# Kernel tuning notes

Measured on AMD Instinct MI355X. Metric: run time of the kernel, lower is better.

## Reference

```python
import jax, jax.numpy as jnp
import numpy as np

# Longformer-base-4096 dims; attention_window=128 -> one-sided window 64
B, S, D, H, L, F, V, NUM_LABELS = 1, 4096, 768, 12, 12, 3072, 50265, 100
DH = D // H
W = 64            # one-sided sliding window
NC = S // W       # number of query chunks
EPS = 1e-5
SCALE = float(1.0 / np.sqrt(DH))


def layer_norm(x, s, b):
    m = jnp.mean(x, axis=-1, keepdims=True)
    v = jnp.mean(jnp.square(x - m), axis=-1, keepdims=True)
    return (x - m) * jax.lax.rsqrt(v + EPS) * s + b


def heads(x):  # [B,S,D] -> [B,H,S,DH]
    return x.reshape(B, S, H, DH).transpose(0, 2, 1, 3)


def chunk3(t):  # [B,H,S,DH] -> [B,H,NC,3W,DH]: key blocks c-1,c,c+1 per query chunk c
    tp = jnp.pad(t, ((0, 0), (0, 0), (W, W), (0, 0)))
    tb = tp.reshape(B, H, NC + 2, W, DH)
    return jnp.concatenate([tb[:, :, i:i + NC] for i in range(3)], axis=3)


def _forward(input_ids, attention_mask, emb_tok, emb_pos, ln_emb_scale, ln_emb_bias,
             Wq, bq, Wk, bk, Wv, bv, Wqg, bqg, Wkg, bkg, Wvg, bvg, Wo, bo,
             ln1_scale, ln1_bias, Wf1, bf1, Wf2, bf2, ln2_scale, ln2_bias, Wc, bc):
    am = attention_mask > 0                      # [B,S]
    x = layer_norm(emb_tok[input_ids] + emb_pos[None, :, :], ln_emb_scale, ln_emb_bias)

    # static sliding-window masks, shared by all layers
    qi = jnp.arange(W)[:, None]
    kj = jnp.arange(3 * W)[None, :]
    band = (kj >= qi) & (kj <= qi + 2 * W)       # |key - query| <= W within a chunk triple
    kvalid = am & (jnp.arange(S)[None, :] > 0)   # global token (pos 0) excluded from window
    kp = jnp.pad(kvalid, ((0, 0), (W, W))).reshape(B, NC + 2, W)
    kmask = jnp.concatenate([kp[:, i:i + NC] for i in range(3)], axis=2)   # [B,NC,3W]
    win_mask = band[None, None, None] & kmask[:, None, :, None, :]         # [B,1,NC,W,3W]

    def layer(x, p):
        (wq, bq_, wk, bk_, wv, bv_, wqg, bqg_, wkg, bkg_, wvg, bvg_, wo, bo_,
         l1s, l1b, wf1, bf1_, wf2, bf2_, l2s, l2b) = p
        q = heads(x @ wq + bq_) * SCALE
        k = heads(x @ wk + bk_)
        v = heads(x @ wv + bv_)
        qc = q.reshape(B, H, NC, W, DH)
        k3, v3 = chunk3(k), chunk3(v)
        sc = jnp.einsum('bhcqd,bhckd->bhcqk', qc, k3)          # [B,H,NC,W,3W]
        sc = jnp.where(win_mask, sc, -1e9)
        # every token also attends to the global CLS key (standard K/V of pos 0)
        sg = jnp.einsum('bhsd,bhd->bhs', q, k[:, :, 0]).reshape(B, H, NC, W, 1)
        probs = jax.nn.softmax(jnp.concatenate([sg, sc], axis=-1), axis=-1)
        pg, pl = probs[..., 0], probs[..., 1:]
        ctx = jnp.einsum('bhcqk,bhckd->bhcqd', pl, v3).reshape(B, H, S, DH)
        ctx = ctx + pg.reshape(B, H, S, 1) * v[:, :, :1]
        # global token attends to everything with its own (global) projections
        qg = heads(x @ wqg + bqg_)[:, :, 0] * SCALE            # [B,H,DH]
        kg = heads(x @ wkg + bkg_)
        vg = heads(x @ wvg + bvg_)
        sgl = jnp.where(am[:, None, :], jnp.einsum('bhd,bhjd->bhj', qg, kg), -1e9)
        ctx0 = jnp.einsum('bhj,bhjd->bhd', jax.nn.softmax(sgl, axis=-1), vg)
        ctx = ctx.at[:, :, 0].set(ctx0)
        attn = ctx.transpose(0, 2, 1, 3).reshape(B, S, D) @ wo + bo_
        x1 = layer_norm(x + attn, l1s, l1b)
        h = jax.nn.gelu(x1 @ wf1 + bf1_, approximate=False)
        return layer_norm(x1 + h @ wf2 + bf2_, l2s, l2b), None

    params = (Wq, bq, Wk, bk, Wv, bv, Wqg, bqg, Wkg, bkg, Wvg, bvg, Wo, bo,
              ln1_scale, ln1_bias, Wf1, bf1, Wf2, bf2, ln2_scale, ln2_bias)
    x, _ = jax.lax.scan(layer, x, params)
    return x[:, 0] @ Wc + bc                                   # [B, NUM_LABELS]


def setup_inputs():
    key = jax.random.key(0)
    ks = jax.random.split(key, 40)
    it = iter(range(40))
    nrm = lambda shape: jax.random.normal(ks[next(it)], shape, dtype=jnp.float32) * 0.02
    z = lambda shape: jnp.zeros(shape, jnp.float32)
    o = lambda shape: jnp.ones(shape, jnp.float32)
    return {
        'input_ids': jax.random.randint(ks[next(it)], (B, S), 0, V, dtype=jnp.int32),
        'attention_mask': jnp.ones((B, S), dtype=jnp.int32),
        'emb_tok': nrm((V, D)), 'emb_pos': nrm((S, D)),
        'ln_emb_scale': o((D,)), 'ln_emb_bias': z((D,)),
        'Wq': nrm((L, D, D)), 'bq': z((L, D)),
        'Wk': nrm((L, D, D)), 'bk': z((L, D)),
        'Wv': nrm((L, D, D)), 'bv': z((L, D)),
        'Wqg': nrm((L, D, D)), 'bqg': z((L, D)),
        'Wkg': nrm((L, D, D)), 'bkg': z((L, D)),
        'Wvg': nrm((L, D, D)), 'bvg': z((L, D)),
        'Wo': nrm((L, D, D)), 'bo': z((L, D)),
        'ln1_scale': o((L, D)), 'ln1_bias': z((L, D)),
        'Wf1': nrm((L, D, F)), 'bf1': z((L, F)),
        'Wf2': nrm((L, F, D)), 'bf2': z((L, D)),
        'ln2_scale': o((L, D)), 'ln2_bias': z((L, D)),
        'Wc': nrm((D, NUM_LABELS)), 'bc': z((NUM_LABELS,)),
    }


def reference(input_ids, attention_mask, emb_tok, emb_pos, ln_emb_scale, ln_emb_bias,
              Wq, bq, Wk, bk, Wv, bv, Wqg, bqg, Wkg, bkg, Wvg, bvg, Wo, bo,
              ln1_scale, ln1_bias, Wf1, bf1, Wf2, bf2, ln2_scale, ln2_bias, Wc, bc):
    return _forward(input_ids, attention_mask, emb_tok, emb_pos, ln_emb_scale, ln_emb_bias,
                    Wq, bq, Wk, bk, Wv, bv, Wqg, bqg, Wkg, bkg, Wvg, bvg, Wo, bo,
                    ln1_scale, ln1_bias, Wf1, bf1, Wf2, bf2, ln2_scale, ln2_bias, Wc, bc)
```

## Files before the change

kernel.cpp:

```cpp
#include <hip/hip_runtime.h>
#include <hip/hip_bf16.h>

typedef unsigned short u16;
typedef __attribute__((ext_vector_type(8))) short bf16x8;
typedef __attribute__((ext_vector_type(4))) float f32x4;

constexpr int S = 4096, D = 768, H = 12, NL = 12, F = 3072, NLAB = 100, DH = 64;
constexpr int NQKV = 3840;
constexpr float SCALE = 0.125f;
constexpr float EPS = 1e-5f;

__device__ __forceinline__ float bits2f(u16 u) {
  union { unsigned int i; float f; } x; x.i = ((unsigned int)u) << 16; return x.f;
}
__device__ __forceinline__ u16 f2bbits(float f) {
  union { float f; unsigned int i; } x; x.f = f;
  return (u16)((x.i + 0x7FFFu + ((x.i >> 16) & 1u)) >> 16);
}
__device__ __forceinline__ float rdw(const void* p, size_t i, int isf32) {
  return isf32 ? ((const float*)p)[i] : bits2f(((const u16*)p)[i]);
}
__device__ __forceinline__ void gload16(const void* g, void* l) {
  __builtin_amdgcn_global_load_lds(
      (const __attribute__((address_space(1))) void*)g,
      (__attribute__((address_space(3))) void*)l, 16, 0, 0);
}

__global__ void detect_k(const void* lns, int* flag) {
  *flag = (*(const unsigned int*)lns == 0x3F800000u) ? 1 : 0;
}

struct PrepArgs {
  const void *Wq, *Wk, *Wv, *Wkg, *Wvg, *Wo, *Wqg, *Wf1, *Wf2;
  const void *bq, *bk, *bv, *bkg, *bvg, *bo, *bqg, *bf1, *bf2;
  u16 *wt_qkv, *wt_o, *wt_qg, *wt_f1, *wt_f2;
  float* biasb;
  const int* flag;
};

__global__ __launch_bounds__(256) void prep_all(PrepArgs a)
{
  const int l = blockIdx.x / 8676;
  const int b = blockIdx.x % 8676;
  const int t = threadIdx.x;
  const int isf32 = *a.flag;
  const size_t oDD = (size_t)l * D * D, oDF = (size_t)l * D * F;
  const size_t oD = (size_t)l * D, oF = (size_t)l * F;
  u16* wqkv = a.wt_qkv + (size_t)l * NQKV * D;
  u16* wo   = a.wt_o   + (size_t)l * D * D;
  u16* wqg  = a.wt_qg  + (size_t)l * D * D;
  u16* wf1  = a.wt_f1  + (size_t)l * F * D;
  u16* wf2  = a.wt_f2  + (size_t)l * D * F;
  float* bb = a.biasb + (size_t)l * 9216;

  if (b < 8640) {
    __shared__ float tile[32][33];
    const void* src; size_t soff; int N, ld, rowoff, n0, k0;
    u16* dst; float scl = 1.f;
    if (b < 4032) {
      const int m = b / 576, ti = b - m * 576;
      soff = oDD; N = D; ld = D; rowoff = 0;
      switch (m) {
        case 0:  src = a.Wq;  dst = wqkv; scl = SCALE;  break;
        case 1:  src = a.Wk;  dst = wqkv; rowoff = 768; break;
        case 2:  src = a.Wv;  dst = wqkv; rowoff = 1536; break;
        case 3:  src = a.Wkg; dst = wqkv; rowoff = 2304; break;
        case 4:  src = a.Wvg; dst = wqkv; rowoff = 3072; break;
        case 5:  src = a.Wo;  dst = wo;   break;
        default: src = a.Wqg; dst = wqg;  scl = SCALE;  break;
      }
      n0 = (ti % 24) * 32; k0 = (ti / 24) * 32;
    } else if (b < 6336) {
      const int ti = b - 4032;
      src = a.Wf1; soff = oDF; N = F; dst = wf1; rowoff = 0; ld = D;
      n0 = (ti % 96) * 32; k0 = (ti / 96) * 32;
    } else {
      const int ti = b - 6336;
      src = a.Wf2; soff = oDF; N = D; dst = wf2; rowoff = 0; ld = F;
      n0 = (ti % 24) * 32; k0 = (ti / 24) * 32;
    }
    const int r = t >> 3, cc = (t & 7) << 2;
    const size_t si = soff + (size_t)(k0 + r) * N + n0 + cc;
    if (isf32) {
      const float4 v = *reinterpret_cast<const float4*>(&((const float*)src)[si]);
      tile[r][cc] = v.x * scl; tile[r][cc+1] = v.y * scl;
      tile[r][cc+2] = v.z * scl; tile[r][cc+3] = v.w * scl;
    } else {
      const ushort4 v = *reinterpret_cast<const ushort4*>(&((const u16*)src)[si]);
      tile[r][cc] = bits2f(v.x) * scl; tile[r][cc+1] = bits2f(v.y) * scl;
      tile[r][cc+2] = bits2f(v.z) * scl; tile[r][cc+3] = bits2f(v.w) * scl;
    }
    __syncthreads();
    const ushort4 ov = make_ushort4(f2bbits(tile[cc+0][r]), f2bbits(tile[cc+1][r]),
                                    f2bbits(tile[cc+2][r]), f2bbits(tile[cc+3][r]));
    *reinterpret_cast<ushort4*>(&dst[(size_t)(rowoff + n0 + r) * ld + k0 + cc]) = ov;
  } else {
    const int i = (b - 8640) * 256 + t;
    float v;
    if      (i < 768)  v = rdw(a.bq,  oD + i,        isf32) * SCALE;
    else if (i < 1536) v = rdw(a.bk,  oD + i - 768,  isf32);
    else if (i < 2304) v = rdw(a.bv,  oD + i - 1536, isf32);
    else if (i < 3072) v = rdw(a.bkg, oD + i - 2304, isf32);
    else if (i < 3840) v = rdw(a.bvg, oD + i - 3072, isf32);
    else if (i < 4608) v = rdw(a.bo,  oD + i - 3840, isf32);
    else if (i < 7680) v = rdw(a.bf1, oF + i - 4608, isf32);
    else if (i < 8448) v = rdw(a.bf2, oD + i - 7680, isf32);
    else               v = rdw(a.bqg, oD + i - 8448, isf32) * SCALE;
    bb[i] = v;
  }
}

template<int BN, int SPLITK>
__global__ __launch_bounds__(256) void mfma_gemm(
    const u16* __restrict__ A, const u16* __restrict__ BT,
    const float* __restrict__ bias,
    float* __restrict__ Cf, u16* __restrict__ Cb,
    int M, int N, int K, int act)
{
  constexpr int BM = 128, BK = 32;
  constexpr int WN = BN / 2;
  constexpr int NR = WN / 16;
  __shared__ u16 As[BM * BK];
  __shared__ u16 Bs[BN * BK];
  const int t = threadIdx.x;
  const int wid = t >> 6, lane = t & 63;
  const int wr = wid >> 1, wc = wid & 1;
  const int m0 = blockIdx.y * BM, n0 = blockIdx.x * BN;
  const int z = (SPLITK > 1) ? blockIdx.z : 0;
  const int kLen = K / SPLITK;
  const int k0 = z * kLen;
  const int l_row = lane >> 2;
  const int l_kc = (lane & 3) << 3;

  f32x4 acc[4][NR];
#pragma unroll
  for (int m = 0; m < 4; ++m)
#pragma unroll
    for (int n = 0; n < NR; ++n)
      acc[m][n] = (f32x4){0.f, 0.f, 0.f, 0.f};

  const int frow = lane & 15;
  const int fkb = (lane >> 4) << 3;

  for (int kt = k0; kt < k0 + kLen; kt += BK) {
#pragma unroll
    for (int i = 0; i < 2; ++i) {
      const int ch = wid * 2 + i;
      gload16(&A[(size_t)(m0 + ch * 16 + l_row) * K + kt + l_kc], &As[ch * 512]);
    }
#pragma unroll
    for (int i = 0; i < BN / 64; ++i) {
      const int ch = wid * (BN / 64) + i;
      gload16(&BT[(size_t)(n0 + ch * 16 + l_row) * K + kt + l_kc], &Bs[ch * 512]);
    }
    __syncthreads();
    bf16x8 af[4], bfr[NR];
#pragma unroll
    for (int m = 0; m < 4; ++m)
      af[m] = *reinterpret_cast<const bf16x8*>(&As[(wr * 64 + m * 16 + frow) * BK + fkb]);
#pragma unroll
    for (int n = 0; n < NR; ++n)
      bfr[n] = *reinterpret_cast<const bf16x8*>(&Bs[(wc * WN + n * 16 + frow) * BK + fkb]);
#pragma unroll
    for (int m = 0; m < 4; ++m)
#pragma unroll
      for (int n = 0; n < NR; ++n)
        acc[m][n] = __builtin_amdgcn_mfma_f32_16x16x32_bf16(af[m], bfr[n], acc[m][n], 0, 0, 0);
    __syncthreads();
  }

  float* Cp = (SPLITK > 1) ? (Cf + (size_t)z * M * N) : Cf;
  const int crow = (lane >> 4) << 2;
  const int ccol = lane & 15;
#pragma unroll
  for (int m = 0; m < 4; ++m) {
#pragma unroll
    for (int n = 0; n < NR; ++n) {
      const int gc = n0 + wc * WN + n * 16 + ccol;
      const float bv = (z == 0) ? bias[gc] : 0.f;
#pragma unroll
      for (int r = 0; r < 4; ++r) {
        const int gr = m0 + wr * 64 + m * 16 + crow + r;
        float x = acc[m][n][r] + bv;
        if (SPLITK == 1 && act) x = 0.5f * x * (1.0f + erff(x * 0.70710678118654752f));
        if (Cp) Cp[(size_t)gr * N + gc] = x;
        if (SPLITK == 1 && Cb) Cb[(size_t)gr * N + gc] = f2bbits(x);
      }
    }
  }
}

__global__ void embed_k(const int* __restrict__ ids, const void* __restrict__ tok,
                        const void* __restrict__ pos, float* __restrict__ out,
                        const int* __restrict__ flag)
{
  const int isf32 = *flag;
  const int s = blockIdx.x, t = threadIdx.x;
  const int id = ids[s];
  for (int c = t; c < D; c += 256)
    out[(size_t)s * D + c] = rdw(tok, (size_t)id * D + c, isf32) + rdw(pos, (size_t)s * D + c, isf32);
}

__global__ __launch_bounds__(256) void ln_res_k(
    const float* __restrict__ Ain,
    const float* __restrict__ P0, const float* __restrict__ P1,
    const float* __restrict__ P2, const float* __restrict__ P3,
    const void* __restrict__ g, size_t goff, const void* __restrict__ b, size_t boff,
    float* __restrict__ Out, u16* __restrict__ Outb, const int* __restrict__ flag)
{
  const int isf32 = *flag;
  const int w = threadIdx.x >> 6, lane = threadIdx.x & 63;
  const int r = blockIdx.x * 4 + w;
  const size_t rb = (size_t)r * D;
  float v[12];
  float ls = 0.f;
#pragma unroll
  for (int j = 0; j < 3; ++j) {
    const int c = lane * 4 + j * 256;
    float4 x = *reinterpret_cast<const float4*>(&Ain[rb + c]);
    if (P0) { const float4 p = *reinterpret_cast<const float4*>(&P0[rb + c]);
              x.x += p.x; x.y += p.y; x.z += p.z; x.w += p.w; }
    if (P1) { const float4 p = *reinterpret_cast<const float4*>(&P1[rb + c]);
              x.x += p.x; x.y += p.y; x.z += p.z; x.w += p.w; }
    if (P2) { const float4 p = *reinterpret_cast<const float4*>(&P2[rb + c]);
              x.x += p.x; x.y += p.y; x.z += p.z; x.w += p.w; }
    if (P3) { const float4 p = *reinterpret_cast<const float4*>(&P3[rb + c]);
              x.x += p.x; x.y += p.y; x.z += p.z; x.w += p.w; }
    v[j*4+0] = x.x; v[j*4+1] = x.y; v[j*4+2] = x.z; v[j*4+3] = x.w;
    ls += x.x + x.y + x.z + x.w;
  }
#pragma unroll
  for (int off = 32; off; off >>= 1) ls += __shfl_xor(ls, off);
  const float mean = ls * (1.0f / D);
  float lv = 0.f;
#pragma unroll
  for (int e = 0; e < 12; ++e) { const float dd = v[e] - mean; lv += dd * dd; }
#pragma unroll
  for (int off = 32; off; off >>= 1) lv += __shfl_xor(lv, off);
  const float rstd = rsqrtf(lv * (1.0f / D) + EPS);
#pragma unroll
  for (int j = 0; j < 3; ++j) {
    const int c = lane * 4 + j * 256;
    float o[4];
#pragma unroll
    for (int e = 0; e < 4; ++e)
      o[e] = (v[j*4+e] - mean) * rstd * rdw(g, goff + c + e, isf32) + rdw(b, boff + c + e, isf32);
    *reinterpret_cast<float4*>(&Out[rb + c]) = make_float4(o[0], o[1], o[2], o[3]);
    if (Outb)
      *reinterpret_cast<ushort4*>(&Outb[rb + c]) =
          make_ushort4(f2bbits(o[0]), f2bbits(o[1]), f2bbits(o[2]), f2bbits(o[3]));
  }
}

__global__ __launch_bounds__(256) void qg_gemv(
    const u16* __restrict__ Xb, const u16* __restrict__ WgT,
    const float* __restrict__ biasb, float* __restrict__ QG)
{
  const int wid = threadIdx.x >> 6, lane = threadIdx.x & 63;
  const int o = blockIdx.x * 4 + wid;
  float a = 0.f;
#pragma unroll
  for (int j = 0; j < 12; ++j) {
    const int k = j * 64 + lane;
    a += bits2f(Xb[k]) * bits2f(WgT[(size_t)o * 768 + k]);
  }
#pragma unroll
  for (int off = 32; off; off >>= 1) a += __shfl_xor(a, off);
  if (lane == 0) QG[o] = a + biasb[8448 + o];
}

__global__ __launch_bounds__(256) void win_attn3(
    const u16* __restrict__ QKV, const int* __restrict__ am, u16* __restrict__ CTXb)
{
  __shared__ u16 Ql[64 * 64];
  __shared__ u16 Kl[224 * 64];
  __shared__ u16 Vt[64 * 232];
  __shared__ int kwin[224];
  const int c = blockIdx.x, h = blockIdx.y;
  const int t = threadIdx.x, w = t >> 6, lane = t & 63;
  const int base = c * 64 - 64, s0 = c * 64;

  for (int i = t; i < 1024; i += 256) {
    const int r = i >> 4, c4 = (i & 15) << 2;
    const ushort4 v = *reinterpret_cast<const ushort4*>(
        &QKV[(size_t)(s0 + r) * NQKV + h * 64 + c4]);
    *reinterpret_cast<ushort4*>((char*)Ql + ((r * 128 + c4 * 2) ^ ((r & 7) << 4))) = v;
  }
  for (int i = t; i < 3584; i += 256) {
    const int r = i >> 4, c4 = (i & 15) << 2;
    const int kp = (r < 192) ? (base + r) : ((r == 192) ? 0 : -1);
    ushort4 v = make_ushort4(0, 0, 0, 0);
    if (kp >= 0 && kp < S)
      v = *reinterpret_cast<const ushort4*>(&QKV[(size_t)kp * NQKV + 768 + h * 64 + c4]);
    *reinterpret_cast<ushort4*>((char*)Kl + ((r * 128 + c4 * 2) ^ ((r & 7) << 4))) = v;
  }
  for (int i = t; i < 3584; i += 256) {
    const int r = i >> 4, c4 = (i & 15) << 2;
    const int kp = (r < 192) ? (base + r) : ((r == 192) ? 0 : -1);
    ushort4 v = make_ushort4(0, 0, 0, 0);
    if (kp >= 0 && kp < S)
      v = *reinterpret_cast<const ushort4*>(&QKV[(size_t)kp * NQKV + 1536 + h * 64 + c4]);
    Vt[(c4 + 0) * 232 + r] = v.x;
    Vt[(c4 + 1) * 232 + r] = v.y;
    Vt[(c4 + 2) * 232 + r] = v.z;
    Vt[(c4 + 3) * 232 + r] = v.w;
  }
  if (t < 224) {
    const int kp = base + t;
    kwin[t] = (t < 192 && kp >= 1 && kp < S) ? am[kp] : 0;
  }
  __syncthreads();

  const int frow = lane & 15, fkb = (lane >> 4) << 3;
  const int crow = (lane >> 4) << 2, ccol = lane & 15;
  const int qrow = w * 16 + frow;

  bf16x8 aq[2];
#pragma unroll
  for (int ks = 0; ks < 2; ++ks)
    aq[ks] = *reinterpret_cast<const bf16x8*>(
        (const char*)Ql + ((qrow * 128 + (ks * 32 + fkb) * 2) ^ ((qrow & 7) << 4)));

  f32x4 sc[14];
#pragma unroll
  for (int tl = 0; tl < 14; ++tl) {
    sc[tl] = (f32x4){0.f, 0.f, 0.f, 0.f};
    const int key = tl * 16 + frow;
#pragma unroll
    for (int ks = 0; ks < 2; ++ks) {
      const bf16x8 bk = *reinterpret_cast<const bf16x8*>(
          (const char*)Kl + ((key * 128 + (ks * 32 + fkb) * 2) ^ ((key & 7) << 4)));
      sc[tl] = __builtin_amdgcn_mfma_f32_16x16x32_bf16(aq[ks], bk, sc[tl], 0, 0, 0);
    }
  }

  float m4[4] = {-1e30f, -1e30f, -1e30f, -1e30f};
#pragma unroll
  for (int tl = 0; tl < 14; ++tl) {
    const int kidx = tl * 16 + ccol;
    const int kw = kwin[kidx];
    const bool isg = (kidx == 192);
#pragma unroll
    for (int r = 0; r < 4; ++r) {
      const int qi = w * 16 + crow + r;
      const bool valid = isg || ((kidx >= qi) && (kidx <= qi + 128) && kw);
      const float v = valid ? sc[tl][r] : -1e30f;
      sc[tl][r] = v;
      m4[r] = fmaxf(m4[r], v);
    }
  }
#pragma unroll
  for (int r = 0; r < 4; ++r)
#pragma unroll
    for (int off = 8; off; off >>= 1) m4[r] = fmaxf(m4[r], __shfl_xor(m4[r], off));

  float ssum[4] = {0.f, 0.f, 0.f, 0.f};
#pragma unroll
  for (int tl = 0; tl < 14; ++tl)
#pragma unroll
    for (int r = 0; r < 4; ++r) {
      const float e = __expf(sc[tl][r] - m4[r]);
      sc[tl][r] = e;
      ssum[r] += e;
    }
#pragma unroll
  for (int r = 0; r < 4; ++r)
#pragma unroll
    for (int off = 8; off; off >>= 1) ssum[r] += __shfl_xor(ssum[r], off);

  __syncthreads();
  u16* Pl = Kl;
#pragma unroll
  for (int tl = 0; tl < 14; ++tl) {
    const int kidx = tl * 16 + ccol;
#pragma unroll
    for (int r = 0; r < 4; ++r) {
      const int row = crow + r;
      *(u16*)((char*)Pl + w * 7168 + ((row * 448 + kidx * 2) ^ ((row & 7) << 4))) =
          f2bbits(sc[tl][r]);
    }
  }
  __syncthreads();

  bf16x8 pa[7];
#pragma unroll
  for (int ks = 0; ks < 7; ++ks)
    pa[ks] = *reinterpret_cast<const bf16x8*>(
        (const char*)Pl + w * 7168 + ((frow * 448 + (ks * 32 + fkb) * 2) ^ ((frow & 7) << 4)));

  f32x4 av[4];
#pragma unroll
  for (int n = 0; n < 4; ++n) {
    av[n] = (f32x4){0.f, 0.f, 0.f, 0.f};
#pragma unroll
    for (int ks = 0; ks < 7; ++ks) {
      const bf16x8 bv = *reinterpret_cast<const bf16x8*>(&Vt[(n * 16 + frow) * 232 + ks * 32 + fkb]);
      av[n] = __builtin_amdgcn_mfma_f32_16x16x32_bf16(pa[ks], bv, av[n], 0, 0, 0);
    }
  }
  float inv[4];
#pragma unroll
  for (int r = 0; r < 4; ++r) inv[r] = 1.f / ssum[r];
#pragma unroll
  for (int n = 0; n < 4; ++n)
#pragma unroll
    for (int r = 0; r < 4; ++r) {
      const int s = s0 + w * 16 + crow + r;
      CTXb[(size_t)s * D + h * 64 + n * 16 + ccol] = f2bbits(av[n][r] * inv[r]);
    }
}

__global__ __launch_bounds__(256) void glob_part(
    const u16* __restrict__ QKV, const float* __restrict__ QG,
    const int* __restrict__ am, float* __restrict__ gp)
{
  __shared__ float qsh[DH];
  __shared__ float se[256];
  __shared__ float red[4];
  __shared__ float part[4][DH];
  const int seg = blockIdx.x, h = blockIdx.y, t = threadIdx.x;
  const int j0 = seg * 256;
  if (t < DH) qsh[t] = QG[h * DH + t];
  __syncthreads();
  const int j = j0 + t;
  float a = 0.f;
  const u16* kr = &QKV[(size_t)j * NQKV + 2304 + h * 64];
#pragma unroll
  for (int v8 = 0; v8 < 8; ++v8) {
    const bf16x8 kv = *reinterpret_cast<const bf16x8*>(&kr[v8 * 8]);
#pragma unroll
    for (int e = 0; e < 8; ++e)
      a += qsh[v8 * 8 + e] * bits2f((u16)kv[e]);
  }
  a = (am[j] > 0) ? a : -1e9f;
  float m = a;
#pragma unroll
  for (int off = 32; off; off >>= 1) m = fmaxf(m, __shfl_xor(m, off));
  if ((t & 63) == 0) red[t >> 6] = m;
  __syncthreads();
  m = fmaxf(fmaxf(red[0], red[1]), fmaxf(red[2], red[3]));
  const float e = __expf(a - m);
  se[t] = e;
  float ls = e;
#pragma unroll
  for (int off = 32; off; off >>= 1) ls += __shfl_xor(ls, off);
  __syncthreads();
  if ((t & 63) == 0) red[t >> 6] = ls;
  __syncthreads();
  const float lsum = red[0] + red[1] + red[2] + red[3];
  const int g = t >> 6, d = t & 63;
  float acc = 0.f;
  for (int jj = g; jj < 256; jj += 4)
    acc += se[jj] * bits2f(QKV[(size_t)(j0 + jj) * NQKV + 3072 + h * 64 + d]);
  part[g][d] = acc;
  __syncthreads();
  if (t < 64) {
    float* o = &gp[(size_t)(h * 16 + seg) * 66];
    o[t] = part[0][t] + part[1][t] + part[2][t] + part[3][t];
    if (t == 0) { o[64] = m; o[65] = lsum; }
  }
}

__global__ void glob_comb(const float* __restrict__ gp, u16* __restrict__ CTXb)
{
  const int h = blockIdx.x, t = threadIdx.x;
  float M = -1e30f;
  for (int i = 0; i < 16; ++i) M = fmaxf(M, gp[(size_t)(h * 16 + i) * 66 + 64]);
  float L = 0.f, acc = 0.f;
  for (int i = 0; i < 16; ++i) {
    const float* o = &gp[(size_t)(h * 16 + i) * 66];
    const float w = __expf(o[64] - M);
    L += o[65] * w;
    acc += o[t] * w;
  }
  CTXb[h * 64 + t] = f2bbits(acc / L);
}

__global__ __launch_bounds__(256) void cls_k(
    const float* __restrict__ X, const void* __restrict__ Wc,
    const void* __restrict__ bc, void* __restrict__ out,
    const int* __restrict__ flag)
{
  const int isf32 = *flag;
  const int wid = threadIdx.x >> 6, lane = threadIdx.x & 63;
  const int n = blockIdx.x * 4 + wid;
  if (n >= NLAB) return;
  float a = 0.f;
#pragma unroll
  for (int j = 0; j < 12; ++j) {
    const int k = j * 64 + lane;
    a += X[k] * rdw(Wc, (size_t)k * NLAB + n, isf32);
  }
#pragma unroll
  for (int off = 32; off; off >>= 1) a += __shfl_xor(a, off);
  if (lane == 0) {
    a += rdw(bc, n, isf32);
    if (isf32) ((float*)out)[n] = a;
    else ((u16*)out)[n] = f2bbits(a);
  }
}

extern "C" void kernel_launch(void* const* d_in, const int* in_sizes, int n_in,
                              void* d_out, int out_size, void* d_ws, size_t ws_size,
                              hipStream_t stream)
{
  const int*  ids = (const int*)d_in[0];
  const int*  am  = (const int*)d_in[1];
  const void* emb_tok = d_in[2];
  const void* emb_pos = d_in[3];
  const void* ln_e_g  = d_in[4];
  const void* ln_e_b  = d_in[5];
  const void* Wq  = d_in[6];  const void* bq  = d_in[7];
  const void* Wk  = d_in[8];  const void* bk  = d_in[9];
  const void* Wv  = d_in[10]; const void* bv  = d_in[11];
  const void* Wqg = d_in[12]; const void* bqg = d_in[13];
  const void* Wkg = d_in[14]; const void* bkg = d_in[15];
  const void* Wvg = d_in[16]; const void* bvg = d_in[17];
  const void* Wo  = d_in[18]; const void* bo  = d_in[19];
  const void* l1g = d_in[20]; const void* l1b = d_in[21];
  const void* Wf1 = d_in[22]; const void* bf1 = d_in[23];
  const void* Wf2 = d_in[24]; const void* bf2 = d_in[25];
  const void* l2g = d_in[26]; const void* l2b = d_in[27];
  const void* Wc  = d_in[28]; const void* bc  = d_in[29];

  float* ws = (float*)d_ws;
  const size_t SD = (size_t)S * D;
  size_t cur = 0;
  auto af32 = [&](size_t n) { float* p = ws + cur; cur += n; return p; };
  auto au16 = [&](size_t n_u16) { u16* p = (u16*)(ws + cur); cur += (n_u16 + 1) / 2; return p; };

  float* X     = af32(SD);
  float* X1    = af32(SD);
  float* TMP   = af32(2 * SD);
  u16*   QKV16 = au16(5 * SD);
  u16*   Hb    = au16((size_t)S * F);
  u16*   Xb    = au16(SD);
  u16*   X1b   = au16(SD);
  u16*   CTXb  = au16(SD);
  u16*   wt_qkv = au16((size_t)NL * NQKV * D);
  u16*   wt_o   = au16((size_t)NL * D * D);
  u16*   wt_qg  = au16((size_t)NL * D * D);
  u16*   wt_f1  = au16((size_t)NL * F * D);
  u16*   wt_f2  = au16((size_t)NL * D * F);
  float* biasb  = af32((size_t)NL * 9216);
  float* QGb    = af32(768);
  float* gp     = af32((size_t)H * 16 * 66);
  int*   flag   = (int*)af32(4);

  float* T0 = TMP;
  float* T1 = TMP + SD;

  detect_k<<<1, 1, 0, stream>>>(ln_e_g, flag);

  PrepArgs pa;
  pa.Wq = Wq; pa.Wk = Wk; pa.Wv = Wv; pa.Wkg = Wkg; pa.Wvg = Wvg;
  pa.Wo = Wo; pa.Wqg = Wqg; pa.Wf1 = Wf1; pa.Wf2 = Wf2;
  pa.bq = bq; pa.bk = bk; pa.bv = bv; pa.bkg = bkg; pa.bvg = bvg;
  pa.bo = bo; pa.bqg = bqg; pa.bf1 = bf1; pa.bf2 = bf2;
  pa.wt_qkv = wt_qkv; pa.wt_o = wt_o; pa.wt_qg = wt_qg;
  pa.wt_f1 = wt_f1; pa.wt_f2 = wt_f2; pa.biasb = biasb; pa.flag = flag;
  prep_all<<<NL * 8676, 256, 0, stream>>>(pa);

  embed_k<<<S, 256, 0, stream>>>(ids, emb_tok, emb_pos, T0, flag);
  ln_res_k<<<S / 4, 256, 0, stream>>>(T0, nullptr, nullptr, nullptr, nullptr,
                                      ln_e_g, 0, ln_e_b, 0, X, Xb, flag);

  for (int l = 0; l < NL; ++l) {
    const size_t oD = (size_t)l * D;
    u16* wqkv_l = wt_qkv + (size_t)l * NQKV * D;
    u16* wo_l   = wt_o   + (size_t)l * D * D;
    u16* wqg_l  = wt_qg  + (size_t)l * D * D;
    u16* wf1_l  = wt_f1  + (size_t)l * F * D;
    u16* wf2_l  = wt_f2  + (size_t)l * D * F;
    float* bb_l = biasb + (size_t)l * 9216;

    mfma_gemm<128, 1><<<dim3(NQKV / 128, S / 128), 256, 0, stream>>>(
        Xb, wqkv_l, bb_l, nullptr, QKV16, S, NQKV, D, 0);
    qg_gemv<<<192, 256, 0, stream>>>(Xb, wqg_l, bb_l, QGb);
    win_attn3<<<dim3(S / 64, H), 256, 0, stream>>>(QKV16, am, CTXb);
    glob_part<<<dim3(16, H), 256, 0, stream>>>(QKV16, QGb, am, gp);
    glob_comb<<<H, 64, 0, stream>>>(gp, CTXb);
    mfma_gemm<64, 2><<<dim3(D / 64, S / 128, 2), 256, 0, stream>>>(
        CTXb, wo_l, bb_l + 3840, TMP, nullptr, S, D, D, 0);
    ln_res_k<<<S / 4, 256, 0, stream>>>(X, T0, T1, nullptr, nullptr,
                                        l1g, oD, l1b, oD, X1, X1b, flag);
    mfma_gemm<128, 1><<<dim3(F / 128, S / 128), 256, 0, stream>>>(
        X1b, wf1_l, bb_l + 4608, nullptr, Hb, S, F, D, 1);
    mfma_gemm<64, 2><<<dim3(D / 64, S / 128, 2), 256, 0, stream>>>(
        Hb, wf2_l, bb_l + 7680, TMP, nullptr, S, D, F, 0);
    ln_res_k<<<S / 4, 256, 0, stream>>>(X1, T0, T1, nullptr, nullptr,
                                        l2g, oD, l2b, oD, X, Xb, flag);
  }
  cls_k<<<25, 256, 0, stream>>>(X, Wc, bc, d_out, flag);
}
```

Baseline: 3.104 ms.

## Fuse global-token attention into one kernel and retile weight prep to 64x64

Three ideas land together. The weight transpose/convert prep kernel now works on 64x64 tiles, converting to bf16 before writing LDS and storing 16-byte vectors, which means four times fewer blocks and wider global writes. The global-query GEMV, the partial global attention and the combine step merge into a single kernel per head with 512 threads, which removes two launches per layer and the intermediate partial buffers. Fusing leaves only 12 blocks doing the global attention, so each block works through all 4096 keys serially and less of the GPU is in use. The unused P2/P3 residual inputs of the layernorm kernel are also dropped.

```diff
diff --git a/kernel.cpp b/kernel.cpp
--- a/kernel.cpp
+++ b/kernel.cpp
@@ -3,6 +3,7 @@
 
 typedef unsigned short u16;
 typedef __attribute__((ext_vector_type(8))) short bf16x8;
+typedef __attribute__((ext_vector_type(8))) unsigned short u16x8;
 typedef __attribute__((ext_vector_type(4))) float f32x4;
 
 constexpr int S = 4096, D = 768, H = 12, NL = 12, F = 3072, NLAB = 100, DH = 64;
@@ -37,65 +38,76 @@
   float* biasb;
   const int* flag;
 };
+constexpr int PPL = 2196;
 
 __global__ __launch_bounds__(256) void prep_all(PrepArgs a)
 {
-  const int l = blockIdx.x / 8676;
-  const int b = blockIdx.x % 8676;
+  const int l = blockIdx.x / PPL;
+  const int b = blockIdx.x % PPL;
   const int t = threadIdx.x;
   const int isf32 = *a.flag;
   const size_t oDD = (size_t)l * D * D, oDF = (size_t)l * D * F;
   const size_t oD = (size_t)l * D, oF = (size_t)l * F;
-  u16* wqkv = a.wt_qkv + (size_t)l * NQKV * D;
-  u16* wo   = a.wt_o   + (size_t)l * D * D;
-  u16* wqg  = a.wt_qg  + (size_t)l * D * D;
-  u16* wf1  = a.wt_f1  + (size_t)l * F * D;
-  u16* wf2  = a.wt_f2  + (size_t)l * D * F;
   float* bb = a.biasb + (size_t)l * 9216;
 
-  if (b < 8640) {
-    __shared__ float tile[32][33];
+  if (b < 2160) {
+    __shared__ u16 tileT[64][72];
     const void* src; size_t soff; int N, ld, rowoff, n0, k0;
     u16* dst; float scl = 1.f;
-    if (b < 4032) {
-      const int m = b / 576, ti = b - m * 576;
+    if (b < 1008) {
+      const int m = b / 144, ti = b % 144;
       soff = oDD; N = D; ld = D; rowoff = 0;
       switch (m) {
-        case 0:  src = a.Wq;  dst = wqkv; scl = SCALE;  break;
-        case 1:  src = a.Wk;  dst = wqkv; rowoff = 768; break;
-        case 2:  src = a.Wv;  dst = wqkv; rowoff = 1536; break;
-        case 3:  src = a.Wkg; dst = wqkv; rowoff = 2304; break;
-        case 4:  src = a.Wvg; dst = wqkv; rowoff = 3072; break;
-        case 5:  src = a.Wo;  dst = wo;   break;
-        default: src = a.Wqg; dst = wqg;  scl = SCALE;  break;
+        case 0:  src = a.Wq;  dst = a.wt_qkv + (size_t)l * NQKV * D; scl = SCALE;  break;
+        case 1:  src = a.Wk;  dst = a.wt_qkv + (size_t)l * NQKV * D; rowoff = 768; break;
+        case 2:  src = a.Wv;  dst = a.wt_qkv + (size_t)l * NQKV * D; rowoff = 1536; break;
+        case 3:  src = a.Wkg; dst = a.wt_qkv + (size_t)l * NQKV * D; rowoff = 2304; break;
+        case 4:  src = a.Wvg; dst = a.wt_qkv + (size_t)l * NQKV * D; rowoff = 3072; break;
+        case 5:  src = a.Wo;  dst = a.wt_o   + (size_t)l * D * D;    break;
+        default: src = a.Wqg; dst = a.wt_qg  + (size_t)l * D * D;    scl = SCALE;  break;
       }
-      n0 = (ti % 24) * 32; k0 = (ti / 24) * 32;
-    } else if (b < 6336) {
-      const int ti = b - 4032;
-      src = a.Wf1; soff = oDF; N = F; dst = wf1; rowoff = 0; ld = D;
-      n0 = (ti % 96) * 32; k0 = (ti / 96) * 32;
+      n0 = (ti % 12) * 64; k0 = (ti / 12) * 64;
+    } else if (b < 1584) {
+      const int ti = b - 1008;
+      src = a.Wf1; soff = oDF; N = F; ld = D; rowoff = 0;
+      dst = a.wt_f1 + (size_t)l * F * D;
+      n0 = (ti % 48) * 64; k0 = (ti / 48) * 64;
     } else {
-      const int ti = b - 6336;
-      src = a.Wf2; soff = oDF; N = D; dst = wf2; rowoff = 0; ld = F;
-      n0 = (ti % 24) * 32; k0 = (ti / 24) * 32;
-    }
-    const int r = t >> 3, cc = (t & 7) << 2;
-    const size_t si = soff + (size_t)(k0 + r) * N + n0 + cc;
-    if (isf32) {
-      const float4 v = *reinterpret_cast<const float4*>(&((const float*)src)[si]);
-      tile[r][cc] = v.x * scl; tile[r][cc+1] = v.y * scl;
-      tile[r][cc+2] = v.z * scl; tile[r][cc+3] = v.w * scl;
-    } else {
-      const ushort4 v = *reinterpret_cast<const ushort4*>(&((const u16*)src)[si]);
-      tile[r][cc] = bits2f(v.x) * scl; tile[r][cc+1] = bits2f(v.y) * scl;
-      tile[r][cc+2] = bits2f(v.z) * scl; tile[r][cc+3] = bits2f(v.w) * scl;
+      const int ti = b - 1584;
+      src = a.Wf2; soff = oDF; N = D; ld = F; rowoff = 0;
+      dst = a.wt_f2 + (size_t)l * D * F;
+      n0 = (ti % 12) * 64; k0 = (ti / 12) * 64;
+    }
+    const int r = t >> 2;
+    const int cb = (t & 3) << 4;
+#pragma unroll
+    for (int u = 0; u < 4; ++u) {
+      const int c = cb + u * 4;
+      const size_t si = soff + (size_t)(k0 + r) * N + n0 + c;
+      float x0, x1, x2, x3;
+      if (isf32) {
+        const float4 v = *reinterpret_cast<const float4*>(&((const float*)src)[si]);
+        x0 = v.x * scl; x1 = v.y * scl; x2 = v.z * scl; x3 = v.w * scl;
+      } else {
+        const ushort4 v = *reinterpret_cast<const ushort4*>(&((const u16*)src)[si]);
+        x0 = bits2f(v.x) * scl; x1 = bits2f(v.y) * scl;
+        x2 = bits2f(v.z) * scl; x3 = bits2f(v.w) * scl;
+      }
+      tileT[c + 0][r] = f2bbits(x0);
+      tileT[c + 1][r] = f2bbits(x1);
+      tileT[c + 2][r] = f2bbits(x2);
+      tileT[c + 3][r] = f2bbits(x3);
     }
     __syncthreads();
-    const ushort4 ov = make_ushort4(f2bbits(tile[cc+0][r]), f2bbits(tile[cc+1][r]),
-                                    f2bbits(tile[cc+2][r]), f2bbits(tile[cc+3][r]));
-    *reinterpret_cast<ushort4*>(&dst[(size_t)(rowoff + n0 + r) * ld + k0 + cc]) = ov;
+    const int n = t >> 2;
+    const int kc = (t & 3) << 4;
+    const u16x8 o0 = *reinterpret_cast<const u16x8*>(&tileT[n][kc]);
+    const u16x8 o1 = *reinterpret_cast<const u16x8*>(&tileT[n][kc + 8]);
+    u16* drow = &dst[(size_t)(rowoff + n0 + n) * ld + k0 + kc];
+    *reinterpret_cast<u16x8*>(drow) = o0;
+    *reinterpret_cast<u16x8*>(drow + 8) = o1;
   } else {
-    const int i = (b - 8640) * 256 + t;
+    const int i = (b - 2160) * 256 + t;
     float v;
     if      (i < 768)  v = rdw(a.bq,  oD + i,        isf32) * SCALE;
     else if (i < 1536) v = rdw(a.bk,  oD + i - 768,  isf32);
@@ -204,7 +216,6 @@
 __global__ __launch_bounds__(256) void ln_res_k(
     const float* __restrict__ Ain,
     const float* __restrict__ P0, const float* __restrict__ P1,
-    const float* __restrict__ P2, const float* __restrict__ P3,
     const void* __restrict__ g, size_t goff, const void* __restrict__ b, size_t boff,
     float* __restrict__ Out, u16* __restrict__ Outb, const int* __restrict__ flag)
 {
@@ -222,10 +233,6 @@
               x.x += p.x; x.y += p.y; x.z += p.z; x.w += p.w; }
     if (P1) { const float4 p = *reinterpret_cast<const float4*>(&P1[rb + c]);
               x.x += p.x; x.y += p.y; x.z += p.z; x.w += p.w; }
-    if (P2) { const float4 p = *reinterpret_cast<const float4*>(&P2[rb + c]);
-              x.x += p.x; x.y += p.y; x.z += p.z; x.w += p.w; }
-    if (P3) { const float4 p = *reinterpret_cast<const float4*>(&P3[rb + c]);
-              x.x += p.x; x.y += p.y; x.z += p.z; x.w += p.w; }
     v[j*4+0] = x.x; v[j*4+1] = x.y; v[j*4+2] = x.z; v[j*4+3] = x.w;
     ls += x.x + x.y + x.z + x.w;
   }
@@ -250,23 +257,6 @@
       *reinterpret_cast<ushort4*>(&Outb[rb + c]) =
           make_ushort4(f2bbits(o[0]), f2bbits(o[1]), f2bbits(o[2]), f2bbits(o[3]));
   }
-}
-
-__global__ __launch_bounds__(256) void qg_gemv(
-    const u16* __restrict__ Xb, const u16* __restrict__ WgT,
-    const float* __restrict__ biasb, float* __restrict__ QG)
-{
-  const int wid = threadIdx.x >> 6, lane = threadIdx.x & 63;
-  const int o = blockIdx.x * 4 + wid;
-  float a = 0.f;
-#pragma unroll
-  for (int j = 0; j < 12; ++j) {
-    const int k = j * 64 + lane;
-    a += bits2f(Xb[k]) * bits2f(WgT[(size_t)o * 768 + k]);
-  }
-#pragma unroll
-  for (int off = 32; off; off >>= 1) a += __shfl_xor(a, off);
-  if (lane == 0) QG[o] = a + biasb[8448 + o];
 }
 
 __global__ __launch_bounds__(256) void win_attn3(
@@ -410,70 +400,84 @@
     }
 }
 
-__global__ __launch_bounds__(256) void glob_part(
-    const u16* __restrict__ QKV, const float* __restrict__ QG,
-    const int* __restrict__ am, float* __restrict__ gp)
-{
-  __shared__ float qsh[DH];
-  __shared__ float se[256];
-  __shared__ float red[4];
-  __shared__ float part[4][DH];
-  const int seg = blockIdx.x, h = blockIdx.y, t = threadIdx.x;
-  const int j0 = seg * 256;
-  if (t < DH) qsh[t] = QG[h * DH + t];
-  __syncthreads();
-  const int j = j0 + t;
-  float a = 0.f;
-  const u16* kr = &QKV[(size_t)j * NQKV + 2304 + h * 64];
-#pragma unroll
-  for (int v8 = 0; v8 < 8; ++v8) {
-    const bf16x8 kv = *reinterpret_cast<const bf16x8*>(&kr[v8 * 8]);
-#pragma unroll
-    for (int e = 0; e < 8; ++e)
-      a += qsh[v8 * 8 + e] * bits2f((u16)kv[e]);
-  }
-  a = (am[j] > 0) ? a : -1e9f;
-  float m = a;
-#pragma unroll
-  for (int off = 32; off; off >>= 1) m = fmaxf(m, __shfl_xor(m, off));
-  if ((t & 63) == 0) red[t >> 6] = m;
-  __syncthreads();
-  m = fmaxf(fmaxf(red[0], red[1]), fmaxf(red[2], red[3]));
-  const float e = __expf(a - m);
-  se[t] = e;
-  float ls = e;
+__global__ __launch_bounds__(512) void glob_attn(
+    const u16* __restrict__ Xb, const u16* __restrict__ WgT,
+    const float* __restrict__ bb, const u16* __restrict__ QKV,
+    const int* __restrict__ am, u16* __restrict__ CTXb)
+{
+  __shared__ float qsh[64];
+  __shared__ float sc[S];
+  __shared__ float red8[8];
+  __shared__ float part[8][64];
+  const int h = blockIdx.x;
+  const int t = threadIdx.x, w = t >> 6, lane = t & 63;
+
+  for (int j = 0; j < 8; ++j) {
+    const int oo = w * 8 + j, o = h * 64 + oo;
+    float a = 0.f;
+#pragma unroll
+    for (int jj = 0; jj < 12; ++jj) {
+      const int k = jj * 64 + lane;
+      a += bits2f(Xb[k]) * bits2f(WgT[(size_t)o * 768 + k]);
+    }
+#pragma unroll
+    for (int off = 32; off; off >>= 1) a += __shfl_xor(a, off);
+    if (lane == 0) qsh[oo] = a + bb[8448 + o];
+  }
+  __syncthreads();
+
+  float s8[8];
+  float lmax = -1e30f;
+#pragma unroll
+  for (int kk = 0; kk < 8; ++kk) {
+    const int j = kk * 512 + t;
+    const u16* kr = &QKV[(size_t)j * NQKV + 2304 + h * 64];
+    float a = 0.f;
+#pragma unroll
+    for (int v8 = 0; v8 < 8; ++v8) {
+      const bf16x8 kv = *reinterpret_cast<const bf16x8*>(&kr[v8 * 8]);
+#pragma unroll
+      for (int e = 0; e < 8; ++e) a += qsh[v8 * 8 + e] * bits2f((u16)kv[e]);
+    }
+    a = (am[j] > 0) ? a : -1e9f;
+    s8[kk] = a;
+    lmax = fmaxf(lmax, a);
+  }
+#pragma unroll
+  for (int off = 32; off; off >>= 1) lmax = fmaxf(lmax, __shfl_xor(lmax, off));
+  if (lane == 0) red8[w] = lmax;
+  __syncthreads();
+  float m = red8[0];
+#pragma unroll
+  for (int i = 1; i < 8; ++i) m = fmaxf(m, red8[i]);
+  __syncthreads();
+
+  float ls = 0.f;
+#pragma unroll
+  for (int kk = 0; kk < 8; ++kk) {
+    const float e = __expf(s8[kk] - m);
+    sc[kk * 512 + t] = e;
+    ls += e;
+  }
 #pragma unroll
   for (int off = 32; off; off >>= 1) ls += __shfl_xor(ls, off);
-  __syncthreads();
-  if ((t & 63) == 0) red[t >> 6] = ls;
-  __syncthreads();
-  const float lsum = red[0] + red[1] + red[2] + red[3];
-  const int g = t >> 6, d = t & 63;
+  if (lane == 0) red8[w] = ls;
+  __syncthreads();
+  float L = 0.f;
+#pragma unroll
+  for (int i = 0; i < 8; ++i) L += red8[i];
+
   float acc = 0.f;
-  for (int jj = g; jj < 256; jj += 4)
-    acc += se[jj] * bits2f(QKV[(size_t)(j0 + jj) * NQKV + 3072 + h * 64 + d]);
-  part[g][d] = acc;
+  for (int j = w; j < S; j += 8)
+    acc += sc[j] * bits2f(QKV[(size_t)j * NQKV + 3072 + h * 64 + lane]);
+  part[w][lane] = acc;
   __syncthreads();
   if (t < 64) {
-    float* o = &gp[(size_t)(h * 16 + seg) * 66];
-    o[t] = part[0][t] + part[1][t] + part[2][t] + part[3][t];
-    if (t == 0) { o[64] = m; o[65] = lsum; }
-  }
-}
-
-__global__ void glob_comb(const float* __restrict__ gp, u16* __restrict__ CTXb)
-{
-  const int h = blockIdx.x, t = threadIdx.x;
-  float M = -1e30f;
-  for (int i = 0; i < 16; ++i) M = fmaxf(M, gp[(size_t)(h * 16 + i) * 66 + 64]);
-  float L = 0.f, acc = 0.f;
-  for (int i = 0; i < 16; ++i) {
-    const float* o = &gp[(size_t)(h * 16 + i) * 66];
-    const float w = __expf(o[64] - M);
-    L += o[65] * w;
-    acc += o[t] * w;
-  }
-  CTXb[h * 64 + t] = f2bbits(acc / L);
+    float s = 0.f;
+#pragma unroll
+    for (int i = 0; i < 8; ++i) s += part[i][t];
+    CTXb[h * 64 + t] = f2bbits(s / L);
+  }
 }
 
 __global__ __launch_bounds__(256) void cls_k(
@@ -543,8 +547,6 @@
   u16*   wt_f1  = au16((size_t)NL * F * D);
   u16*   wt_f2  = au16((size_t)NL * D * F);
   float* biasb  = af32((size_t)NL * 9216);
-  float* QGb    = af32(768);
-  float* gp     = af32((size_t)H * 16 * 66);
   int*   flag   = (int*)af32(4);
 
   float* T0 = TMP;
@@ -559,10 +561,10 @@
   pa.bo = bo; pa.bqg = bqg; pa.bf1 = bf1; pa.bf2 = bf2;
   pa.wt_qkv = wt_qkv; pa.wt_o = wt_o; pa.wt_qg = wt_qg;
   pa.wt_f1 = wt_f1; pa.wt_f2 = wt_f2; pa.biasb = biasb; pa.flag = flag;
-  prep_all<<<NL * 8676, 256, 0, stream>>>(pa);
+  prep_all<<<NL * PPL, 256, 0, stream>>>(pa);
 
   embed_k<<<S, 256, 0, stream>>>(ids, emb_tok, emb_pos, T0, flag);
-  ln_res_k<<<S / 4, 256, 0, stream>>>(T0, nullptr, nullptr, nullptr, nullptr,
+  ln_res_k<<<S / 4, 256, 0, stream>>>(T0, nullptr, nullptr,
                                       ln_e_g, 0, ln_e_b, 0, X, Xb, flag);
 
   for (int l = 0; l < NL; ++l) {
@@ -576,19 +578,17 @@
 
     mfma_gemm<128, 1><<<dim3(NQKV / 128, S / 128), 256, 0, stream>>>(
         Xb, wqkv_l, bb_l, nullptr, QKV16, S, NQKV, D, 0);
-    qg_gemv<<<192, 256, 0, stream>>>(Xb, wqg_l, bb_l, QGb);
     win_attn3<<<dim3(S / 64, H), 256, 0, stream>>>(QKV16, am, CTXb);
-    glob_part<<<dim3(16, H), 256, 0, stream>>>(QKV16, QGb, am, gp);
-    glob_comb<<<H, 64, 0, stream>>>(gp, CTXb);
+    glob_attn<<<H, 512, 0, stream>>>(Xb, wqg_l, bb_l, QKV16, am, CTXb);
     mfma_gemm<64, 2><<<dim3(D / 64, S / 128, 2), 256, 0, stream>>>(
         CTXb, wo_l, bb_l + 3840, TMP, nullptr, S, D, D, 0);
-    ln_res_k<<<S / 4, 256, 0, stream>>>(X, T0, T1, nullptr, nullptr,
+    ln_res_k<<<S / 4, 256, 0, stream>>>(X, T0, T1,
                                         l1g, oD, l1b, oD, X1, X1b, flag);
     mfma_gemm<128, 1><<<dim3(F / 128, S / 128), 256, 0, stream>>>(
         X1b, wf1_l, bb_l + 4608, nullptr, Hb, S, F, D, 1);
     mfma_gemm<64, 2><<<dim3(D / 64, S / 128, 2), 256, 0, stream>>>(
         Hb, wf2_l, bb_l + 7680, TMP, nullptr, S, D, F, 0);
-    ln_res_k<<<S / 4, 256, 0, stream>>>(X1, T0, T1, nullptr, nullptr,
+    ln_res_k<<<S / 4, 256, 0, stream>>>(X1, T0, T1,
                                         l2g, oD, l2b, oD, X, Xb, flag);
   }
   cls_k<<<25, 256, 0, stream>>>(X, Wc, bc, d_out, flag);
```

New measurement: 4.786 ms. +54.2%, slower.
